# Performance work log

Hardware: AMD Instinct MI355X
Metric: run time of the kernel (lower is better)

The kernel has to match this reference:

```python
import jax, jax.numpy as jnp
import numpy as np

EPS = 1e-6
B, CIN, COUT, N, S, M1, M2 = 4, 32, 32, 8192, 8, 12, 12
X, Y = 2 * M1 + 1, 2 * M2 + 1


def setup_inputs() -> dict:
    key = jax.random.key(0)
    ks = jax.random.split(key, 20)
    x = jax.random.normal(ks[0], (B, CIN, N), dtype=jnp.float32)
    loc = jax.random.uniform(ks[1], (B, N, 2), dtype=jnp.float32)
    # per-batch permutation of point indices; equal-size subdomains of N//S points
    ind = jnp.stack([jax.random.permutation(k, N) for k in jax.random.split(ks[2], B)]).astype(jnp.int32)
    ss = 1.0 / S
    sc = 1.0 / (CIN * COUT)
    u = lambda k, shp, s: s * jax.random.uniform(k, shp, dtype=jnp.float32)
    inp = {
        'x': x, 'loc': loc, 'ind': ind,
        'w1s_re': u(ks[3], (S, X, M2), ss), 'w1s_im': u(ks[4], (S, X, M2), ss),
        'w2s_re': u(ks[5], (S, M1 + 1, 1), ss), 'w2s_im': u(ks[6], (S, M1 + 1, 1), ss),
        'w1_re': u(ks[7], (CIN, COUT, X, M2), sc), 'w1_im': u(ks[8], (CIN, COUT, X, M2), sc),
        'w2_re': u(ks[9], (CIN, COUT, M1 + 1, 1), sc), 'w2_im': u(ks[10], (CIN, COUT, M1 + 1, 1), sc),
        'w1sb_re': u(ks[11], (S, X, M2), ss), 'w1sb_im': u(ks[12], (S, X, M2), ss),
        'w2sb_re': u(ks[13], (S, M1 + 1, 1), ss), 'w2sb_im': u(ks[14], (S, M1 + 1, 1), ss),
    }
    return inp


def _forward(x, loc, ind, w1s, w2s, w1, w2, w1sb, w2sb):
    b, cin, n = x.shape
    s, xg_dim, m2 = w1s.shape
    m1 = (xg_dim - 1) // 2
    xx, yy = 2 * m1 + 1, 2 * m2 + 1
    p = n // s
    norm = jnp.asarray(1.0 / np.sqrt(xx * yy), jnp.float32)

    # gather per-subdomain points (equal partitions replace the sep ragged split)
    xg = jnp.take_along_axis(x, ind[:, None, :], axis=2).reshape(b, cin, s, p)
    locg = jnp.take_along_axis(loc, ind[:, :, None], axis=1).reshape(b, s, p, 2)

    # per-subdomain min-max normalization of coords to [-pi, pi]
    om = jnp.swapaxes(locg, -1, -2)                      # [b,s,2,p]
    om = om - om.min(-1, keepdims=True)
    om = om / (om.max(-1, keepdims=True) + EPS)
    om = om * (2.0 * jnp.pi) - jnp.pi

    kx = (jnp.arange(xx) - m1).astype(jnp.float32)
    ky = (jnp.arange(yy) - m2).astype(jnp.float32)
    # exact (type-1) NUDFT basis; conj-wrapped adjoint = sum_p d_p exp(-i k.omega_p)
    E1 = jnp.exp(-1j * om[:, :, 0, :, None] * kx)        # [b,s,p,X]
    E2 = jnp.exp(-1j * om[:, :, 1, :, None] * ky)        # [b,s,p,Y]

    coef = jnp.einsum('bcsp,bspx,bspy->bcsxy', xg.astype(jnp.complex64), E1, E2) * norm

    i1 = coef[..., :m2]                                  # [b,c,s,X,m2]
    i2 = coef[:, :, :, :m1 + 1, m2:m2 + 1]               # [b,c,s,m1+1,1]

    i1 = jnp.einsum('bisxy,sxy->bixy', i1, w1s)
    i2 = jnp.einsum('bisxy,sxy->bixy', i2, w2s)
    i1 = jnp.einsum('bixy,ioxy->boxy', i1, w1)
    i2 = jnp.einsum('bixy,ioxy->boxy', i2, w2)
    i1 = jnp.einsum('boxy,sxy->bosxy', i1, w1sb)
    i2 = jnp.einsum('boxy,sxy->bosxy', i2, w2sb)

    cout = i1.shape[1]
    full = jnp.zeros((b, cout, s, xx, yy), jnp.complex64)
    full = full.at[..., :m2].set(i1)
    full = full.at[..., yy - m2:].set(jnp.conj(i1[..., ::-1, ::-1]))
    full = full.at[..., xx - m1 - 1:, m2:m2 + 1].set(jnp.conj(i2[..., ::-1, ::-1]))
    full = full.at[..., :m1 + 1, m2:m2 + 1].set(i2)      # overwrites center row (mode 0)

    # conj-wrapped forward NUFFT: sum_k c_k exp(+i k.omega_p)
    outc = jnp.einsum('bcsxy,bspx,bspy->bcsp', full, jnp.conj(E1), jnp.conj(E2)) * norm
    outr = outc.real                                     # [b,cout,s,p]

    # per-subdomain min-max renormalization back to input data range
    t = outr - outr.min(-1, keepdims=True)
    t = t / (t.max(-1, keepdims=True) + EPS)
    mn = xg.min(-1, keepdims=True)
    mx = xg.max(-1, keepdims=True)
    vals = t * (mx - mn) + mn                            # needs cin == cout

    # scatter back: output[b,:,ind[b,j]] = vals[b,:,j]
    inv = jnp.argsort(ind, axis=1)
    return jnp.take_along_axis(vals.reshape(b, cout, n), inv[:, None, :], axis=2)


def reference(x, loc, ind, w1s_re, w1s_im, w2s_re, w2s_im, w1_re, w1_im,
              w2_re, w2_im, w1sb_re, w1sb_im, w2sb_re, w2sb_im):
    c = lambda re, im: (re + 1j * im).astype(jnp.complex64)
    return _forward(x, loc, ind, c(w1s_re, w1s_im), c(w2s_re, w2s_im),
                    c(w1_re, w1_im), c(w2_re, w2_im),
                    c(w1sb_re, w1sb_im), c(w2sb_re, w2sb_im))
```

## Files before the change

kernel.cpp:

```cpp
#include <hip/hip_runtime.h>

#define B_ 4
#define C_ 32
#define N_ 8192
#define S_ 8
#define P_ 1024
#define NM_FWD 325
#define NM_INV 313
#define NORM_F 0.04f

#define PI_F 3.14159265358979f
#define TWOPI_F 6.28318530717959f

__device__ __forceinline__ float blk_red(float v, float* red, bool is_min){
  int tid = threadIdx.x;
  red[tid] = v; __syncthreads();
  for (int off = blockDim.x >> 1; off > 0; off >>= 1){
    if (tid < off) red[tid] = is_min ? fminf(red[tid], red[tid+off]) : fmaxf(red[tid], red[tid+off]);
    __syncthreads();
  }
  float r = red[0]; __syncthreads();
  return r;
}

__global__ __launch_bounds__(256) void k_om(const float* __restrict__ loc,
                                            const int* __restrict__ ind,
                                            float* __restrict__ om){
  int b = blockIdx.x >> 3, s = blockIdx.x & 7;
  int tid = threadIdx.x;
  __shared__ float l0[P_], l1[P_];
  __shared__ float red[256];
  const int* indb = ind + b*N_ + s*P_;
  float mn0=1e30f, mx0=-1e30f, mn1=1e30f, mx1=-1e30f;
  for (int p = tid; p < P_; p += 256){
    int n = indb[p];
    float a = loc[(b*N_ + n)*2];
    float c = loc[(b*N_ + n)*2 + 1];
    l0[p] = a; l1[p] = c;
    mn0 = fminf(mn0, a); mx0 = fmaxf(mx0, a);
    mn1 = fminf(mn1, c); mx1 = fmaxf(mx1, c);
  }
  mn0 = blk_red(mn0, red, true);  mx0 = blk_red(mx0, red, false);
  mn1 = blk_red(mn1, red, true);  mx1 = blk_red(mx1, red, false);
  float i0 = TWOPI_F / (mx0 - mn0 + 1e-6f);
  float i1 = TWOPI_F / (mx1 - mn1 + 1e-6f);
  float* om0 = om + ((b*S_ + s)*2)*P_;
  float* om1 = om0 + P_;
  for (int p = tid; p < P_; p += 256){
    om0[p] = (l0[p] - mn0)*i0 - PI_F;
    om1[p] = (l1[p] - mn1)*i1 - PI_F;
  }
}

__global__ __launch_bounds__(512) void k_xg(const float* __restrict__ x,
                                            const int* __restrict__ ind,
                                            float* __restrict__ xg_t,
                                            float* __restrict__ pmm){
  int blk = blockIdx.x;
  int part = blk & 3, bs = blk >> 2;
  int b = bs >> 3, s = bs & 7;
  int t = threadIdx.x;
  int c = t & 31, pl = t >> 5;
  __shared__ int inds[256];
  __shared__ float rmn[8*32], rmx[8*32];
  if (t < 256) inds[t] = ind[b*N_ + s*P_ + part*256 + t];
  __syncthreads();
  const float* xr = x + (b*C_ + c)*N_;
  float mn = 1e30f, mx = -1e30f;
  int pbase = part*256;
  #pragma unroll 4
  for (int k = 0; k < 16; ++k){
    int pp = pl + k*16;
    float v = xr[inds[pp]];
    xg_t[(bs*P_ + pbase + pp)*C_ + c] = v;
    mn = fminf(mn, v); mx = fmaxf(mx, v);
  }
  mn = fminf(mn, __shfl_xor(mn, 32));
  mx = fmaxf(mx, __shfl_xor(mx, 32));
  int wid = t >> 6;
  if ((t & 63) < 32){ rmn[wid*32 + c] = mn; rmx[wid*32 + c] = mx; }
  __syncthreads();
  if (t < 32){
    float m0 = rmn[t], M0 = rmx[t];
    #pragma unroll
    for (int w = 1; w < 8; ++w){ m0 = fminf(m0, rmn[w*32+t]); M0 = fmaxf(M0, rmx[w*32+t]); }
    pmm[((bs*4 + part)*32 + t)*2]     = m0;
    pmm[((bs*4 + part)*32 + t)*2 + 1] = M0;
  }
}

__global__ __launch_bounds__(256) void k_wt(
    const float* __restrict__ w1s_re, const float* __restrict__ w1s_im,
    const float* __restrict__ w2s_re, const float* __restrict__ w2s_im,
    const float* __restrict__ w1_re,  const float* __restrict__ w1_im,
    const float* __restrict__ w2_re,  const float* __restrict__ w2_im,
    const float* __restrict__ w1sb_re,const float* __restrict__ w1sb_im,
    const float* __restrict__ w2sb_re,const float* __restrict__ w2sb_im,
    float* __restrict__ w1t, float* __restrict__ w1st, float* __restrict__ w1sbt){
  int q = blockIdx.x;
  int t = threadIdx.x;
  bool p1 = (q < 300);
  int x = p1 ? q % 25 : q - 300;
  int y = p1 ? q / 25 : 12;
  for (int idx = t; idx < 1024; idx += 256){
    float wre, wim;
    if (p1){ int wi = (idx*25 + x)*12 + y; wre = w1_re[wi]; wim = w1_im[wi]; }
    else   { int wi = idx*13 + x;          wre = w2_re[wi]; wim = w2_im[wi]; }
    w1t[(size_t)(q*1024 + idx)*2]     = wre;
    w1t[(size_t)(q*1024 + idx)*2 + 1] = wim;
  }
  if (t < 8){
    int s = t;
    float a, b2, c2, d2;
    if (p1){ int wi = (s*25+x)*12+y; a=w1s_re[wi]; b2=w1s_im[wi]; c2=w1sb_re[wi]; d2=w1sb_im[wi]; }
    else   { int wi = s*13+x;        a=w2s_re[wi]; b2=w2s_im[wi]; c2=w2sb_re[wi]; d2=w2sb_im[wi]; }
    w1st[(q*8+s)*2]   = a;  w1st[(q*8+s)*2+1]  = b2;
    w1sbt[(q*8+s)*2]  = c2; w1sbt[(q*8+s)*2+1] = d2;
  }
}

__global__ __launch_bounds__(448) void k_fwd(const float* __restrict__ om,
                                             const float* __restrict__ xg_t,
                                             float* __restrict__ coef_part){
  int blk = blockIdx.x;
  int part = blk & 1;
  int tile = (blk >> 1) % 6;
  int bs   = blk / 12;
  int t = threadIdx.x;
  int ml = t >> 3;
  int q  = t & 7;
  int mf = tile*56 + ml;
  int mfc = min(mf, NM_FWD-1);
  int xo = mfc / 13, yo = mfc - xo*13;
  float kx = (float)(xo - 12), ky = (float)(yo - 12);
  __shared__ float o0s[512], o1s[512];
  __shared__ __align__(16) float xgs[64*32];
  __shared__ float Wre[56*68], Wim[56*68];
  const float* om0 = om + bs*2*P_;
  const float* om1 = om0 + P_;
  for (int i = t; i < 512; i += 448){
    o0s[i] = om0[part*512 + i];
    o1s[i] = om1[part*512 + i];
  }
  float ar[4] = {0,0,0,0}, ai[4] = {0,0,0,0};
  for (int ch = 0; ch < 8; ++ch){
    int pbase = part*512 + ch*64;
    __syncthreads();
    for (int i = t; i < 512; i += 448){
      ((float4*)xgs)[i] = ((const float4*)xg_t)[(bs*P_ + pbase + (i>>3))*8 + (i&7)];
    }
    {
      int ps = t & 7;
      #pragma unroll
      for (int k = 0; k < 8; ++k){
        int p = ps + k*8;
        float th = o0s[ch*64 + p]*kx + o1s[ch*64 + p]*ky;
        float sn, cs; __sincosf(th, &sn, &cs);
        Wre[ml*68 + p] = cs;
        Wim[ml*68 + p] = sn;
      }
    }
    __syncthreads();
    #pragma unroll 8
    for (int p = 0; p < 64; ++p){
      float4 g4 = *(const float4*)&xgs[p*32 + q*4];
      float wre = Wre[ml*68 + p], wim = Wim[ml*68 + p];
      ar[0] += g4.x*wre; ai[0] += g4.x*wim;
      ar[1] += g4.y*wre; ai[1] += g4.y*wim;
      ar[2] += g4.z*wre; ai[2] += g4.z*wim;
      ar[3] += g4.w*wre; ai[3] += g4.w*wim;
    }
  }
  if (mf < NM_FWD){
    float* dst = coef_part + (size_t)((part*32 + bs)*NM_FWD + mf)*64 + q*8;
    #pragma unroll
    for (int j = 0; j < 4; ++j){
      dst[j*2]     = ar[j]*NORM_F;
      dst[j*2 + 1] = -ai[j]*NORM_F;
    }
  }
}

__global__ __launch_bounds__(64) void k_mid(const float* __restrict__ coef_part,
    const float* __restrict__ w1t, const float* __restrict__ w1st,
    const float* __restrict__ w1sbt, float* __restrict__ zbuf){
  int blk = blockIdx.x;
  int b = blk / NM_INV, q = blk - b*NM_INV;
  int lane = threadIdx.x;
  int o = lane & 31;
  int hi = lane >> 5;
  bool p1 = (q < 300);
  int x = p1 ? q % 25 : q - 300;
  int y = p1 ? q / 25 : 12;
  int mf = x*13 + y;
  __shared__ float iv[64];
  float are = 0.f, aim = 0.f;
  #pragma unroll
  for (int s = 0; s < 8; ++s){
    const float* cp = coef_part + (size_t)((hi*32 + b*8 + s)*NM_FWD + mf)*64 + o*2;
    float cre = cp[0], cim = cp[1];
    float wre = w1st[(q*8+s)*2], wim = w1st[(q*8+s)*2+1];
    are += cre*wre - cim*wim;
    aim += cre*wim + cim*wre;
  }
  are += __shfl_xor(are, 32);
  aim += __shfl_xor(aim, 32);
  if (hi == 0){ iv[o*2] = are; iv[o*2+1] = aim; }
  __syncthreads();
  float ore = 0.f, oim = 0.f;
  #pragma unroll
  for (int ii = 0; ii < 16; ++ii){
    int i = hi*16 + ii;
    float zre = iv[i*2], zim = iv[i*2+1];
    const float* wp = w1t + (size_t)(q*1024 + i*32 + o)*2;
    float wre = wp[0], wim = wp[1];
    ore += zre*wre - zim*wim;
    oim += zre*wim + zim*wre;
  }
  ore += __shfl_xor(ore, 32);
  oim += __shfl_xor(oim, 32);
  float scale = p1 ? 0.08f : ((x==12) ? 0.04f : 0.08f);
  #pragma unroll
  for (int si = 0; si < 4; ++si){
    int s = hi*4 + si;
    float wre = w1sbt[(q*8+s)*2], wim = w1sbt[(q*8+s)*2+1];
    float zre = (ore*wre - oim*wim)*scale;
    float zim = (ore*wim + oim*wre)*scale;
    size_t oi = (size_t)((b*8 + s)*NM_INV + q)*64 + o*2;
    zbuf[oi] = zre; zbuf[oi+1] = zim;
  }
}

__global__ __launch_bounds__(256) void k_inv(const float* __restrict__ om,
                                             const float* __restrict__ zbuf,
                                             float* __restrict__ routc){
  int blk = blockIdx.x;
  int pt = blk & 15, bs = blk >> 4;
  int p0 = pt*64;
  int t = threadIdx.x;
  int oq = t >> 6, pl = t & 63;
  __shared__ __align__(16) float Zs[64*64];
  const float* zb = zbuf + (size_t)bs*NM_INV*64;
  float o0 = om[bs*2*P_ + p0 + pl];
  float o1 = om[bs*2*P_ + P_ + p0 + pl];
  float d0s, d0c; __sincosf(o0, &d0s, &d0c);
  float d1s, d1c; __sincosf(o1, &d1s, &d1c);
  float rs0, rc0; __sincosf(12.f*(o0+o1), &rs0, &rc0);
  float rre = rc0, rim = -rs0;
  float fre = rre, fim = rim;
  int rowc = 0;
  float acc[8] = {0,0,0,0,0,0,0,0};
  for (int chv = 0; chv < 5; ++chv){
    int m0 = chv*64;
    int mcount = min(64, NM_INV - m0);
    __syncthreads();
    for (int i = t*4; i < mcount*64; i += 1024)
      *(float4*)&Zs[i] = *(const float4*)&zb[m0*64 + i];
    __syncthreads();
    const float* zrow = Zs + oq*16;
    for (int m = 0; m < mcount; ++m){
      if (rowc == 25){
        float nr = rre*d1c - rim*d1s;
        float ni = rre*d1s + rim*d1c;
        rre = nr; rim = ni;
        fre = rre; fim = rim;
        rowc = 0;
      }
      float4 za = *(const float4*)&zrow[m*64];
      float4 zb4 = *(const float4*)&zrow[m*64 + 4];
      float4 zc = *(const float4*)&zrow[m*64 + 8];
      float4 zd = *(const float4*)&zrow[m*64 + 12];
      acc[0] += za.x*fre  - za.y*fim;
      acc[1] += za.z*fre  - za.w*fim;
      acc[2] += zb4.x*fre - zb4.y*fim;
      acc[3] += zb4.z*fre - zb4.w*fim;
      acc[4] += zc.x*fre  - zc.y*fim;
      acc[5] += zc.z*fre  - zc.w*fim;
      acc[6] += zd.x*fre  - zd.y*fim;
      acc[7] += zd.z*fre  - zd.w*fim;
      float nf = fre*d0c - fim*d0s;
      float ni = fre*d0s + fim*d0c;
      fre = nf; fim = ni;
      ++rowc;
    }
  }
  float* outp = routc + (size_t)(bs*C_ + oq*8)*P_ + p0 + pl;
  #pragma unroll
  for (int j = 0; j < 8; ++j)
    outp[(size_t)j*P_] = acc[j];
}

__global__ __launch_bounds__(256) void k_fin(const float* __restrict__ routc,
                                             const float* __restrict__ pmm,
                                             const int* __restrict__ ind,
                                             float* __restrict__ out){
  int blk = blockIdx.x;
  int o = blk & 31, s = (blk >> 5) & 7, b = blk >> 8;
  int bs = b*8 + s;
  int t = threadIdx.x;
  __shared__ float red[256];
  const float* rr = routc + (size_t)(bs*C_ + o)*P_;
  float v[4]; float mn = 1e30f, mx = -1e30f;
  #pragma unroll
  for (int k = 0; k < 4; ++k){
    v[k] = rr[t + k*256];
    mn = fminf(mn, v[k]); mx = fmaxf(mx, v[k]);
  }
  mn = blk_red(mn, red, true);
  mx = blk_red(mx, red, false);
  float xmn = 1e30f, xmx = -1e30f;
  #pragma unroll
  for (int part = 0; part < 4; ++part){
    xmn = fminf(xmn, pmm[((bs*4+part)*32 + o)*2]);
    xmx = fmaxf(xmx, pmm[((bs*4+part)*32 + o)*2 + 1]);
  }
  float scale = (xmx - xmn) / (mx - mn + 1e-6f);
  const int* indb = ind + b*N_ + s*P_;
  float* outb = out + (size_t)(b*C_ + o)*N_;
  #pragma unroll
  for (int k = 0; k < 4; ++k){
    int p = t + k*256;
    outb[indb[p]] = (v[k] - mn)*scale + xmn;
  }
}

extern "C" void kernel_launch(void* const* d_in, const int* in_sizes, int n_in,
                              void* d_out, int out_size, void* d_ws, size_t ws_size,
                              hipStream_t stream){
  const float* x      = (const float*)d_in[0];
  const float* loc    = (const float*)d_in[1];
  const int*   ind    = (const int*)  d_in[2];
  const float* w1s_re = (const float*)d_in[3];
  const float* w1s_im = (const float*)d_in[4];
  const float* w2s_re = (const float*)d_in[5];
  const float* w2s_im = (const float*)d_in[6];
  const float* w1_re  = (const float*)d_in[7];
  const float* w1_im  = (const float*)d_in[8];
  const float* w2_re  = (const float*)d_in[9];
  const float* w2_im  = (const float*)d_in[10];
  const float* w1sb_re= (const float*)d_in[11];
  const float* w1sb_im= (const float*)d_in[12];
  const float* w2sb_re= (const float*)d_in[13];
  const float* w2sb_im= (const float*)d_in[14];
  float* out = (float*)d_out;

  float* ws = (float*)d_ws;
  float* om        = ws;
  float* xg_t      = om + 65536;
  float* pmm       = xg_t + 1048576;
  float* coef_part = pmm + 8192;
  float* zbuf      = coef_part + 1331200;
  float* w1t       = zbuf + 641024;
  float* w1st      = w1t + 641024;
  float* w1sbt     = w1st + 5008;
  float* routc     = xg_t;

  k_om <<<32,   256, 0, stream>>>(loc, ind, om);
  k_xg <<<128,  512, 0, stream>>>(x, ind, xg_t, pmm);
  k_wt <<<NM_INV, 256, 0, stream>>>(w1s_re, w1s_im, w2s_re, w2s_im,
                                    w1_re, w1_im, w2_re, w2_im,
                                    w1sb_re, w1sb_im, w2sb_re, w2sb_im,
                                    w1t, w1st, w1sbt);
  k_fwd<<<384,  448, 0, stream>>>(om, xg_t, coef_part);
  k_mid<<<4*NM_INV, 64, 0, stream>>>(coef_part, w1t, w1st, w1sbt, zbuf);
  k_inv<<<512,  256, 0, stream>>>(om, zbuf, routc);
  k_fin<<<1024, 256, 0, stream>>>(routc, pmm, ind, out);
}
```

Before: 209.6 us.

## Pack gathered inputs and spectral coefficients as bf16, restructure forward/inverse NUDFT kernels

Stores the gathered point values and the mid-stage spectral coefficients as packed bf16 pairs, which halves their memory traffic. The forward NUDFT becomes one wavefront per block, where each lane owns one mode and computes its sincos inline over 128 points with 32 channel accumulators. It no longer builds a shared twiddle table, and the point range is split into 8 partial sums that k_mid must now reduce. k_inv gives each thread two points to reuse the Z loads, and k_mid packs four modes per block. Rounding to bf16 lowers precision, and the 64 accumulators per lane may raise register pressure.

New measurement: 232.8 us. +11.1%, slower.

```diff
diff --git a/kernel.cpp b/kernel.cpp
--- a/kernel.cpp
+++ b/kernel.cpp
@@ -11,6 +11,15 @@
 
 #define PI_F 3.14159265358979f
 #define TWOPI_F 6.28318530717959f
+
+__device__ __forceinline__ unsigned pk_bf16(float a, float b){
+  unsigned ab = __float_as_uint(a), bb = __float_as_uint(b);
+  ab = (ab + 0x7FFFu + ((ab >> 16) & 1u)) >> 16;
+  bb = (bb + 0x7FFFu + ((bb >> 16) & 1u)) & 0xFFFF0000u;
+  return ab | bb;
+}
+#define UNPK_LO(u) __uint_as_float((u) << 16)
+#define UNPK_HI(u) __uint_as_float((u) & 0xFFFF0000u)
 
 __device__ __forceinline__ float blk_red(float v, float* red, bool is_min){
   int tid = threadIdx.x;
@@ -54,7 +63,7 @@
 
 __global__ __launch_bounds__(512) void k_xg(const float* __restrict__ x,
                                             const int* __restrict__ ind,
-                                            float* __restrict__ xg_t,
+                                            unsigned* __restrict__ xg_b,
                                             float* __restrict__ pmm){
   int blk = blockIdx.x;
   int part = blk & 3, bs = blk >> 2;
@@ -72,7 +81,9 @@
   for (int k = 0; k < 16; ++k){
     int pp = pl + k*16;
     float v = xr[inds[pp]];
-    xg_t[(bs*P_ + pbase + pp)*C_ + c] = v;
+    float vp = __shfl_xor(v, 1);
+    if ((c & 1) == 0)
+      xg_b[(size_t)(bs*P_ + pbase + pp)*16 + (c >> 1)] = pk_bf16(v, vp);
     mn = fminf(mn, v); mx = fmaxf(mx, v);
   }
   mn = fminf(mn, __shfl_xor(mn, 32));
@@ -119,99 +130,103 @@
   }
 }
 
-__global__ __launch_bounds__(448) void k_fwd(const float* __restrict__ om,
-                                             const float* __restrict__ xg_t,
-                                             float* __restrict__ coef_part){
-  int blk = blockIdx.x;
-  int part = blk & 1;
-  int tile = (blk >> 1) % 6;
-  int bs   = blk / 12;
-  int t = threadIdx.x;
-  int ml = t >> 3;
-  int q  = t & 7;
-  int mf = tile*56 + ml;
-  int mfc = min(mf, NM_FWD-1);
-  int xo = mfc / 13, yo = mfc - xo*13;
+__global__ __launch_bounds__(64) void k_fwd(const float* __restrict__ om,
+                                            const unsigned* __restrict__ xg_b,
+                                            float* __restrict__ coef_part){
+  int blk = blockIdx.x;
+  int pp = blk & 7;
+  int mc = (blk >> 3) % 6;
+  int bs = blk / 48;
+  int lane = threadIdx.x;
+  int m = mc*64 + lane;
+  int mcl = min(m, NM_FWD-1);
+  int xo = mcl / 13, yo = mcl - xo*13;
   float kx = (float)(xo - 12), ky = (float)(yo - 12);
-  __shared__ float o0s[512], o1s[512];
-  __shared__ __align__(16) float xgs[64*32];
-  __shared__ float Wre[56*68], Wim[56*68];
-  const float* om0 = om + bs*2*P_;
-  const float* om1 = om0 + P_;
-  for (int i = t; i < 512; i += 448){
-    o0s[i] = om0[part*512 + i];
-    o1s[i] = om1[part*512 + i];
-  }
-  float ar[4] = {0,0,0,0}, ai[4] = {0,0,0,0};
-  for (int ch = 0; ch < 8; ++ch){
-    int pbase = part*512 + ch*64;
-    __syncthreads();
-    for (int i = t; i < 512; i += 448){
-      ((float4*)xgs)[i] = ((const float4*)xg_t)[(bs*P_ + pbase + (i>>3))*8 + (i&7)];
+  int p0 = pp*128;
+  __shared__ unsigned xs[128*16];
+  __shared__ float2 oms[128];
+  {
+    const uint4* src = (const uint4*)(xg_b + (size_t)(bs*P_ + p0)*16);
+    for (int i = lane; i < 512; i += 64) ((uint4*)xs)[i] = src[i];
+    const float* o0p = om + bs*2*P_ + p0;
+    const float* o1p = o0p + P_;
+    for (int i = lane; i < 128; i += 64) oms[i] = make_float2(o0p[i], o1p[i]);
+  }
+  __syncthreads();
+  float ar[32], ai[32];
+  #pragma unroll
+  for (int c = 0; c < 32; ++c){ ar[c] = 0.f; ai[c] = 0.f; }
+  for (int p = 0; p < 128; ++p){
+    float2 o = oms[p];
+    float th = o.x*kx + o.y*ky;
+    float sn, cs; __sincosf(th, &sn, &cs);
+    const unsigned* xp = &xs[p*16];
+    #pragma unroll
+    for (int j4 = 0; j4 < 4; ++j4){
+      uint4 g = *(const uint4*)&xp[j4*4];
+      int cb = j4*8;
+      float c0 = UNPK_LO(g.x), c1 = UNPK_HI(g.x);
+      float c2 = UNPK_LO(g.y), c3 = UNPK_HI(g.y);
+      float c4 = UNPK_LO(g.z), c5 = UNPK_HI(g.z);
+      float c6 = UNPK_LO(g.w), c7 = UNPK_HI(g.w);
+      ar[cb+0] += c0*cs; ai[cb+0] += c0*sn;
+      ar[cb+1] += c1*cs; ai[cb+1] += c1*sn;
+      ar[cb+2] += c2*cs; ai[cb+2] += c2*sn;
+      ar[cb+3] += c3*cs; ai[cb+3] += c3*sn;
+      ar[cb+4] += c4*cs; ai[cb+4] += c4*sn;
+      ar[cb+5] += c5*cs; ai[cb+5] += c5*sn;
+      ar[cb+6] += c6*cs; ai[cb+6] += c6*sn;
+      ar[cb+7] += c7*cs; ai[cb+7] += c7*sn;
     }
-    {
-      int ps = t & 7;
-      #pragma unroll
-      for (int k = 0; k < 8; ++k){
-        int p = ps + k*8;
-        float th = o0s[ch*64 + p]*kx + o1s[ch*64 + p]*ky;
-        float sn, cs; __sincosf(th, &sn, &cs);
-        Wre[ml*68 + p] = cs;
-        Wim[ml*68 + p] = sn;
-      }
+  }
+  if (m < NM_FWD){
+    float* dst = coef_part + (size_t)((pp*32 + bs)*NM_FWD + m)*64;
+    #pragma unroll
+    for (int c = 0; c < 32; c += 2){
+      *(float4*)&dst[c*2] = make_float4(ar[c]*NORM_F,   -ai[c]*NORM_F,
+                                        ar[c+1]*NORM_F, -ai[c+1]*NORM_F);
     }
-    __syncthreads();
-    #pragma unroll 8
-    for (int p = 0; p < 64; ++p){
-      float4 g4 = *(const float4*)&xgs[p*32 + q*4];
-      float wre = Wre[ml*68 + p], wim = Wim[ml*68 + p];
-      ar[0] += g4.x*wre; ai[0] += g4.x*wim;
-      ar[1] += g4.y*wre; ai[1] += g4.y*wim;
-      ar[2] += g4.z*wre; ai[2] += g4.z*wim;
-      ar[3] += g4.w*wre; ai[3] += g4.w*wim;
-    }
-  }
-  if (mf < NM_FWD){
-    float* dst = coef_part + (size_t)((part*32 + bs)*NM_FWD + mf)*64 + q*8;
-    #pragma unroll
-    for (int j = 0; j < 4; ++j){
-      dst[j*2]     = ar[j]*NORM_F;
-      dst[j*2 + 1] = -ai[j]*NORM_F;
-    }
-  }
-}
-
-__global__ __launch_bounds__(64) void k_mid(const float* __restrict__ coef_part,
+  }
+}
+
+__global__ __launch_bounds__(256) void k_mid(const float* __restrict__ coef_part,
     const float* __restrict__ w1t, const float* __restrict__ w1st,
-    const float* __restrict__ w1sbt, float* __restrict__ zbuf){
-  int blk = blockIdx.x;
-  int b = blk / NM_INV, q = blk - b*NM_INV;
-  int lane = threadIdx.x;
+    const float* __restrict__ w1sbt, unsigned* __restrict__ zpk){
+  int blk = blockIdx.x;
+  int b = blk / 79, qg = blk - b*79;
+  int t = threadIdx.x;
+  int w = t >> 6;
+  int q = min(qg*4 + w, NM_INV-1);
+  int lane = t & 63;
   int o = lane & 31;
   int hi = lane >> 5;
   bool p1 = (q < 300);
   int x = p1 ? q % 25 : q - 300;
   int y = p1 ? q / 25 : 12;
   int mf = x*13 + y;
-  __shared__ float iv[64];
+  __shared__ float iv[4][64];
   float are = 0.f, aim = 0.f;
   #pragma unroll
-  for (int s = 0; s < 8; ++s){
-    const float* cp = coef_part + (size_t)((hi*32 + b*8 + s)*NM_FWD + mf)*64 + o*2;
-    float cre = cp[0], cim = cp[1];
-    float wre = w1st[(q*8+s)*2], wim = w1st[(q*8+s)*2+1];
-    are += cre*wre - cim*wim;
-    aim += cre*wim + cim*wre;
+  for (int ppl = 0; ppl < 4; ++ppl){
+    int pp = hi*4 + ppl;
+    #pragma unroll
+    for (int s = 0; s < 8; ++s){
+      const float* cp = coef_part + (size_t)((pp*32 + b*8 + s)*NM_FWD + mf)*64 + o*2;
+      float cre = cp[0], cim = cp[1];
+      float wre = w1st[(q*8+s)*2], wim = w1st[(q*8+s)*2+1];
+      are += cre*wre - cim*wim;
+      aim += cre*wim + cim*wre;
+    }
   }
   are += __shfl_xor(are, 32);
   aim += __shfl_xor(aim, 32);
-  if (hi == 0){ iv[o*2] = are; iv[o*2+1] = aim; }
+  if (hi == 0){ iv[w][o*2] = are; iv[w][o*2+1] = aim; }
   __syncthreads();
   float ore = 0.f, oim = 0.f;
   #pragma unroll
   for (int ii = 0; ii < 16; ++ii){
     int i = hi*16 + ii;
-    float zre = iv[i*2], zim = iv[i*2+1];
+    float zre = iv[w][i*2], zim = iv[w][i*2+1];
     const float* wp = w1t + (size_t)(q*1024 + i*32 + o)*2;
     float wre = wp[0], wim = wp[1];
     ore += zre*wre - zim*wim;
@@ -226,68 +241,84 @@
     float wre = w1sbt[(q*8+s)*2], wim = w1sbt[(q*8+s)*2+1];
     float zre = (ore*wre - oim*wim)*scale;
     float zim = (ore*wim + oim*wre)*scale;
-    size_t oi = (size_t)((b*8 + s)*NM_INV + q)*64 + o*2;
-    zbuf[oi] = zre; zbuf[oi+1] = zim;
-  }
-}
-
-__global__ __launch_bounds__(256) void k_inv(const float* __restrict__ om,
-                                             const float* __restrict__ zbuf,
+    zpk[(size_t)((b*8 + s)*NM_INV + q)*32 + o] = pk_bf16(zre, zim);
+  }
+}
+
+__global__ __launch_bounds__(128) void k_inv(const float* __restrict__ om,
+                                             const unsigned* __restrict__ zpk,
                                              float* __restrict__ routc){
   int blk = blockIdx.x;
-  int pt = blk & 15, bs = blk >> 4;
-  int p0 = pt*64;
-  int t = threadIdx.x;
-  int oq = t >> 6, pl = t & 63;
-  __shared__ __align__(16) float Zs[64*64];
-  const float* zb = zbuf + (size_t)bs*NM_INV*64;
-  float o0 = om[bs*2*P_ + p0 + pl];
-  float o1 = om[bs*2*P_ + P_ + p0 + pl];
-  float d0s, d0c; __sincosf(o0, &d0s, &d0c);
-  float d1s, d1c; __sincosf(o1, &d1s, &d1c);
-  float rs0, rc0; __sincosf(12.f*(o0+o1), &rs0, &rc0);
-  float rre = rc0, rim = -rs0;
-  float fre = rre, fim = rim;
+  int pt = blk & 7;
+  int oqp = (blk >> 3) & 1;
+  int bs = blk >> 4;
+  int t = threadIdx.x;
+  int w = t >> 6, lane = t & 63;
+  int oq = oqp*2 + w;
+  int p0 = pt*128;
+  __shared__ unsigned zs[64*32];
+  float o0A = om[bs*2*P_ + p0 + lane];
+  float o1A = om[bs*2*P_ + P_ + p0 + lane];
+  float o0B = om[bs*2*P_ + p0 + lane + 64];
+  float o1B = om[bs*2*P_ + P_ + p0 + lane + 64];
+  float d0sA, d0cA; __sincosf(o0A, &d0sA, &d0cA);
+  float d1sA, d1cA; __sincosf(o1A, &d1sA, &d1cA);
+  float d0sB, d0cB; __sincosf(o0B, &d0sB, &d0cB);
+  float d1sB, d1cB; __sincosf(o1B, &d1sB, &d1cB);
+  float rsA, rcA; __sincosf(12.f*(o0A+o1A), &rsA, &rcA);
+  float rsB, rcB; __sincosf(12.f*(o0B+o1B), &rsB, &rcB);
+  float rreA = rcA, rimA = -rsA, rreB = rcB, rimB = -rsB;
+  float freA = rreA, fimA = rimA, freB = rreB, fimB = rimB;
   int rowc = 0;
-  float acc[8] = {0,0,0,0,0,0,0,0};
+  float accA[8] = {0,0,0,0,0,0,0,0};
+  float accB[8] = {0,0,0,0,0,0,0,0};
+  const unsigned* zb = zpk + (size_t)bs*NM_INV*32;
   for (int chv = 0; chv < 5; ++chv){
     int m0 = chv*64;
     int mcount = min(64, NM_INV - m0);
     __syncthreads();
-    for (int i = t*4; i < mcount*64; i += 1024)
-      *(float4*)&Zs[i] = *(const float4*)&zb[m0*64 + i];
+    for (int i = t*4; i < mcount*32; i += 512)
+      *(uint4*)&zs[i] = *(const uint4*)&zb[m0*32 + i];
     __syncthreads();
-    const float* zrow = Zs + oq*16;
     for (int m = 0; m < mcount; ++m){
       if (rowc == 25){
-        float nr = rre*d1c - rim*d1s;
-        float ni = rre*d1s + rim*d1c;
-        rre = nr; rim = ni;
-        fre = rre; fim = rim;
+        float nrA = rreA*d1cA - rimA*d1sA, niA = rreA*d1sA + rimA*d1cA;
+        rreA = nrA; rimA = niA; freA = rreA; fimA = rimA;
+        float nrB = rreB*d1cB - rimB*d1sB, niB = rreB*d1sB + rimB*d1cB;
+        rreB = nrB; rimB = niB; freB = rreB; fimB = rimB;
         rowc = 0;
       }
-      float4 za = *(const float4*)&zrow[m*64];
-      float4 zb4 = *(const float4*)&zrow[m*64 + 4];
-      float4 zc = *(const float4*)&zrow[m*64 + 8];
-      float4 zd = *(const float4*)&zrow[m*64 + 12];
-      acc[0] += za.x*fre  - za.y*fim;
-      acc[1] += za.z*fre  - za.w*fim;
-      acc[2] += zb4.x*fre - zb4.y*fim;
-      acc[3] += zb4.z*fre - zb4.w*fim;
-      acc[4] += zc.x*fre  - zc.y*fim;
-      acc[5] += zc.z*fre  - zc.w*fim;
-      acc[6] += zd.x*fre  - zd.y*fim;
-      acc[7] += zd.z*fre  - zd.w*fim;
-      float nf = fre*d0c - fim*d0s;
-      float ni = fre*d0s + fim*d0c;
-      fre = nf; fim = ni;
+      uint4 ga = *(const uint4*)&zs[m*32 + oq*8];
+      uint4 gb = *(const uint4*)&zs[m*32 + oq*8 + 4];
+      float re0 = UNPK_LO(ga.x), im0 = UNPK_HI(ga.x);
+      float re1 = UNPK_LO(ga.y), im1 = UNPK_HI(ga.y);
+      float re2 = UNPK_LO(ga.z), im2 = UNPK_HI(ga.z);
+      float re3 = UNPK_LO(ga.w), im3 = UNPK_HI(ga.w);
+      float re4 = UNPK_LO(gb.x), im4 = UNPK_HI(gb.x);
+      float re5 = UNPK_LO(gb.y), im5 = UNPK_HI(gb.y);
+      float re6 = UNPK_LO(gb.z), im6 = UNPK_HI(gb.z);
+      float re7 = UNPK_LO(gb.w), im7 = UNPK_HI(gb.w);
+      accA[0] += re0*freA - im0*fimA;  accB[0] += re0*freB - im0*fimB;
+      accA[1] += re1*freA - im1*fimA;  accB[1] += re1*freB - im1*fimB;
+      accA[2] += re2*freA - im2*fimA;  accB[2] += re2*freB - im2*fimB;
+      accA[3] += re3*freA - im3*fimA;  accB[3] += re3*freB - im3*fimB;
+      accA[4] += re4*freA - im4*fimA;  accB[4] += re4*freB - im4*fimB;
+      accA[5] += re5*freA - im5*fimA;  accB[5] += re5*freB - im5*fimB;
+      accA[6] += re6*freA - im6*fimA;  accB[6] += re6*freB - im6*fimB;
+      accA[7] += re7*freA - im7*fimA;  accB[7] += re7*freB - im7*fimB;
+      float nfA = freA*d0cA - fimA*d0sA, niA = freA*d0sA + fimA*d0cA;
+      freA = nfA; fimA = niA;
+      float nfB = freB*d0cB - fimB*d0sB, niB = freB*d0sB + fimB*d0cB;
+      freB = nfB; fimB = niB;
       ++rowc;
     }
   }
-  float* outp = routc + (size_t)(bs*C_ + oq*8)*P_ + p0 + pl;
-  #pragma unroll
-  for (int j = 0; j < 8; ++j)
-    outp[(size_t)j*P_] = acc[j];
+  float* outp = routc + (size_t)(bs*C_ + oq*8)*P_ + p0 + lane;
+  #pragma unroll
+  for (int j = 0; j < 8; ++j){
+    outp[(size_t)j*P_]      = accA[j];
+    outp[(size_t)j*P_ + 64] = accB[j];
+  }
 }
 
 __global__ __launch_bounds__(256) void k_fin(const float* __restrict__ routc,
@@ -345,24 +376,24 @@
   float* out = (float*)d_out;
 
   float* ws = (float*)d_ws;
-  float* om        = ws;
-  float* xg_t      = om + 65536;
-  float* pmm       = xg_t + 1048576;
-  float* coef_part = pmm + 8192;
-  float* zbuf      = coef_part + 1331200;
-  float* w1t       = zbuf + 641024;
-  float* w1st      = w1t + 641024;
-  float* w1sbt     = w1st + 5008;
-  float* routc     = xg_t;
+  float*    om        = ws;
+  unsigned* xg_b      = (unsigned*)(om + 65536);
+  float*    pmm       = (float*)(xg_b + 524288);
+  float*    coef_part = pmm + 8192;
+  unsigned* zpk       = (unsigned*)(coef_part + 5324800);
+  float*    w1t       = (float*)(zpk + 320512);
+  float*    w1st      = w1t + 641024;
+  float*    w1sbt     = w1st + 5008;
+  float*    routc     = coef_part;
 
   k_om <<<32,   256, 0, stream>>>(loc, ind, om);
-  k_xg <<<128,  512, 0, stream>>>(x, ind, xg_t, pmm);
+  k_xg <<<128,  512, 0, stream>>>(x, ind, xg_b, pmm);
   k_wt <<<NM_INV, 256, 0, stream>>>(w1s_re, w1s_im, w2s_re, w2s_im,
                                     w1_re, w1_im, w2_re, w2_im,
                                     w1sb_re, w1sb_im, w2sb_re, w2sb_im,
                                     w1t, w1st, w1sbt);
-  k_fwd<<<384,  448, 0, stream>>>(om, xg_t, coef_part);
-  k_mid<<<4*NM_INV, 64, 0, stream>>>(coef_part, w1t, w1st, w1sbt, zbuf);
-  k_inv<<<512,  256, 0, stream>>>(om, zbuf, routc);
+  k_fwd<<<1536, 64,  0, stream>>>(om, xg_b, coef_part);
+  k_mid<<<316,  256, 0, stream>>>(coef_part, w1t, w1st, w1sbt, zpk);
+  k_inv<<<512,  128, 0, stream>>>(om, zpk, routc);
   k_fin<<<1024, 256, 0, stream>>>(routc, pmm, ind, out);
 }
```
